# Kernel tuning notes

Measured on AMD Instinct MI355X. Metric: run time of the kernel, lower is better.

Reference implementation:

```python
import jax, jax.numpy as jnp
import numpy as np
import math

B, S, E, H = 2, 2048, 1024, 16
D = E // H  # head_size = 64
EPS = 1e-5

def _ln(x, g, b):
    mu = jnp.mean(x, axis=-1, keepdims=True)
    var = jnp.mean(jnp.square(x - mu), axis=-1, keepdims=True)
    return (x - mu) * jax.lax.rsqrt(var + EPS) * g + b

def setup_inputs() -> dict:
    key = jax.random.key(0)
    ks = jax.random.split(key, 16)
    s = 0.02
    return {
        "I": jax.random.normal(ks[0], (B, S, E), jnp.float32),
        "x": jax.random.normal(ks[1], (B, S, E), jnp.float32),
        "mask": jnp.ones((B, 1, S), jnp.int32),
        # per-head Q/K/V weights stacked over heads [H, E, D], biases [H, D]
        "wq": jax.random.normal(ks[2], (H, E, D), jnp.float32) * s,
        "bq": jax.random.normal(ks[3], (H, D), jnp.float32) * s,
        "wk": jax.random.normal(ks[4], (H, E, D), jnp.float32) * s,
        "bk": jax.random.normal(ks[5], (H, D), jnp.float32) * s,
        "wv": jax.random.normal(ks[6], (H, E, D), jnp.float32) * s,
        "bv": jax.random.normal(ks[7], (H, D), jnp.float32) * s,
        "w_proj": jax.random.normal(ks[8], (E, E), jnp.float32) * s,
        "b_proj": jnp.zeros((E,), jnp.float32),
        "g1": jnp.ones((E,), jnp.float32),
        "be1": jnp.zeros((E,), jnp.float32),
        "g2": jnp.ones((E,), jnp.float32),
        "be2": jnp.zeros((E,), jnp.float32),
        "w1": jax.random.normal(ks[9], (E, 4 * E), jnp.float32) * s,
        "b1": jnp.zeros((4 * E,), jnp.float32),
        "w2": jax.random.normal(ks[10], (4 * E, E), jnp.float32) * s,
        "b2": jnp.zeros((E,), jnp.float32),
    }

def reference(I, x, mask, wq, bq, wk, bk, wv, bv, w_proj, b_proj,
              g1, be1, g2, be2, w1, b1, w2, b2):
    xn = _ln(x, g1, be1)
    # batched per-head projections: [B,S,E] x [H,E,D] -> [B,H,S,D]
    q = jnp.einsum('bse,hed->bhsd', I, wq) + bq[None, :, None, :]
    k = jnp.einsum('bse,hed->bhsd', xn, wk) + bk[None, :, None, :]
    v = jnp.einsum('bse,hed->bhsd', xn, wv) + bv[None, :, None, :]
    # NOTE: original scales by sqrt(n_embed), not sqrt(head_size)
    scores = jnp.einsum('bhqd,bhkd->bhqk', q, k) / math.sqrt(E)
    scores = jnp.where(mask[:, None, :, :] == 0, -1e9, scores)
    attn = jax.nn.softmax(scores, axis=-1)
    ctx = jnp.einsum('bhqk,bhkd->bhqd', attn, v)
    # concat heads: [B,S,H,D] -> [B,S,E]
    ctx = ctx.transpose(0, 2, 1, 3).reshape(B, S, E)
    attn_out = ctx @ w_proj + b_proj
    h = xn + attn_out
    h2 = _ln(h, g2, be2)
    ff = jax.nn.gelu(h2 @ w1 + b1, approximate=False) @ w2 + b2
    return h2 + ff
```

## Files before the change

kernel.cpp:

```cpp
#include <hip/hip_runtime.h>
#include <hip/hip_bf16.h>
#include <math.h>

typedef short short8 __attribute__((ext_vector_type(8)));
typedef short short4_t __attribute__((ext_vector_type(4)));
typedef float f32x4 __attribute__((ext_vector_type(4)));
typedef unsigned short u16;
typedef unsigned int u32;

#define B_ 2
#define S_ 2048
#define E_ 1024
#define H_ 16
#define D_ 64
#define TOK (B_*S_)

__device__ __forceinline__ float bf2f(u16 u) {
    union { unsigned int u; float f; } v; v.u = ((unsigned int)u) << 16; return v.f;
}
__device__ __forceinline__ u16 f2bf(float f) {
    union { float f; unsigned int u; } v; v.f = f;
    unsigned int r = v.u + 0x7fffu + ((v.u >> 16) & 1u);
    return (u16)(r >> 16);
}
__device__ __forceinline__ u32 fbits(float f) {
    union { float f; u32 u; } v; v.f = f; return v.u;
}
__device__ __forceinline__ void gl_lds16(const u16* g, short* l) {
    __builtin_amdgcn_global_load_lds(
        (const __attribute__((address_space(1))) unsigned int*)(g),
        (__attribute__((address_space(3))) unsigned int*)(l), 16, 0, 0);
}

__global__ __launch_bounds__(256) void convf_k(const float* __restrict__ s, u16* __restrict__ d)
{
    size_t i = ((size_t)blockIdx.x * 256 + threadIdx.x) * 8;
    f32x4 a = *(const f32x4*)(s + i);
    f32x4 b = *(const f32x4*)(s + i + 4);
    short8 r;
#pragma unroll
    for (int j = 0; j < 4; j++) { r[j] = (short)f2bf(a[j]); r[4 + j] = (short)f2bf(b[j]); }
    *(short8*)(d + i) = r;
}

__global__ __launch_bounds__(256) void tconv_k(
    const float* __restrict__ src, u16* __restrict__ dst,
    int K, int N, size_t zsrc, size_t zdst)
{
    __shared__ u16 t[64][72];
    src += (size_t)blockIdx.z * zsrc;
    dst += (size_t)blockIdx.z * zdst;
    int k0 = blockIdx.y * 64, n0 = blockIdx.x * 64;
    int tid = threadIdx.x;
    int kr = tid >> 4, nc = (tid & 15) * 4;
#pragma unroll
    for (int i = 0; i < 4; i++) {
        f32x4 v = *(const f32x4*)(src + (size_t)(k0 + kr + i * 16) * N + n0 + nc);
#pragma unroll
        for (int j = 0; j < 4; j++) t[kr + i * 16][nc + j] = f2bf(v[j]);
    }
    __syncthreads();
    int nr = tid >> 2, kg = (tid & 3) * 16;
    short8 r0, r1;
#pragma unroll
    for (int j = 0; j < 8; j++) { r0[j] = (short)t[kg + j][nr]; r1[j] = (short)t[kg + 8 + j][nr]; }
    u16* dp = dst + (size_t)(n0 + nr) * K + k0 + kg;
    *(short8*)(dp) = r0;
    *(short8*)(dp + 8) = r1;
}

__global__ __launch_bounds__(256) void tconvqkv_k(
    const float* __restrict__ wq, const float* __restrict__ wk,
    const float* __restrict__ wv, u16* __restrict__ dst)
{
    __shared__ u16 t[64][72];
    int z = blockIdx.z;
    int w = z >> 4, hh = z & 15;
    const float* src = (w == 0 ? wq : (w == 1 ? wk : wv)) + (size_t)hh * E_ * D_;
    u16* d = dst + (size_t)w * E_ * E_ + (size_t)hh * D_ * E_;
    int k0 = blockIdx.y * 64;
    int tid = threadIdx.x;
    int kr = tid >> 4, nc = (tid & 15) * 4;
#pragma unroll
    for (int i = 0; i < 4; i++) {
        f32x4 v = *(const f32x4*)(src + (size_t)(k0 + kr + i * 16) * D_ + nc);
#pragma unroll
        for (int j = 0; j < 4; j++) t[kr + i * 16][nc + j] = f2bf(v[j]);
    }
    __syncthreads();
    int nr = tid >> 2, kg = (tid & 3) * 16;
    short8 r0, r1;
#pragma unroll
    for (int j = 0; j < 8; j++) { r0[j] = (short)t[kg + j][nr]; r1[j] = (short)t[kg + 8 + j][nr]; }
    u16* dp = d + (size_t)nr * E_ + k0 + kg;
    *(short8*)(dp) = r0;
    *(short8*)(dp + 8) = r1;
}

__global__ __launch_bounds__(256) void vtrans_k(const u16* __restrict__ V, u16* __restrict__ Vt)
{
    __shared__ u16 t[64][72];
    int s0 = blockIdx.x * 64, h = blockIdx.y, b = blockIdx.z;
    int tid = threadIdx.x;
    int sr = tid >> 2, dc = (tid & 3) * 16;
    const u16* src = V + (size_t)b * S_ * E_ + (size_t)(s0 + sr) * E_ + h * D_ + dc;
    short8 v0 = *(const short8*)(src);
    short8 v1 = *(const short8*)(src + 8);
#pragma unroll
    for (int j = 0; j < 8; j++) { t[sr][dc + j] = v0[j]; t[sr][dc + 8 + j] = v1[j]; }
    __syncthreads();
    int dr = tid >> 2, sc = (tid & 3) * 16;
    short8 r0, r1;
#pragma unroll
    for (int j = 0; j < 8; j++) { r0[j] = (short)t[sc + j][dr]; r1[j] = (short)t[sc + 8 + j][dr]; }
    u16* dp = Vt + ((size_t)(b * H_ + h) * D_ + dr) * S_ + s0 + sc;
    *(short8*)(dp) = r0;
    *(short8*)(dp + 8) = r1;
}

__global__ __launch_bounds__(256) void maskprep_k(
    const int* __restrict__ mask, float* __restrict__ fb, int* __restrict__ ok)
{
    __shared__ unsigned char fl[256];
    int b = blockIdx.x;
    int tid = threadIdx.x;
    int base = tid * 8;
    unsigned all = 1;
#pragma unroll
    for (int j = 0; j < 8; j++) {
        int m = mask[b * S_ + base + j];
        fb[b * S_ + base + j] = m ? 0.f : -1e9f;
        all &= (m != 0) ? 1u : 0u;
    }
    fl[tid] = (unsigned char)all;
    __syncthreads();
    if (tid < 32) {
        unsigned a = 1;
#pragma unroll
        for (int j = 0; j < 8; j++) a &= fl[tid * 8 + j];
        ok[b * 32 + tid] = (int)a;
    }
}

template<int INF32>
__global__ __launch_bounds__(256) void ln_kernel(
    const void* __restrict__ xv, const float* __restrict__ g,
    const float* __restrict__ be, u16* __restrict__ y)
{
    int lane = threadIdx.x & 63, wave = threadIdx.x >> 6;
    int row = blockIdx.x * 4 + wave;
    int c0 = lane * 16;
    float v[16];
    if (INF32) {
        const float* xr = (const float*)xv + (size_t)row * E_ + c0;
#pragma unroll
        for (int i = 0; i < 4; i++) {
            f32x4 xx = *(const f32x4*)(xr + i * 4);
#pragma unroll
            for (int j = 0; j < 4; j++) v[i * 4 + j] = xx[j];
        }
    } else {
        const u16* xr = (const u16*)xv + (size_t)row * E_ + c0;
        short8 a = *(const short8*)(xr);
        short8 b = *(const short8*)(xr + 8);
#pragma unroll
        for (int j = 0; j < 8; j++) { v[j] = bf2f((u16)a[j]); v[8 + j] = bf2f((u16)b[j]); }
    }
    float s = 0.f, q = 0.f;
#pragma unroll
    for (int i = 0; i < 16; i++) { s += v[i]; q += v[i] * v[i]; }
#pragma unroll
    for (int off = 1; off < 64; off <<= 1) {
        s += __shfl_xor(s, off, 64);
        q += __shfl_xor(q, off, 64);
    }
    float mu = s * (1.0f / E_);
    float var = q * (1.0f / E_) - mu * mu;
    float rstd = rsqrtf(var + 1e-5f);
    u16* yr = y + (size_t)row * E_ + c0;
    short8 o0, o1;
#pragma unroll
    for (int j = 0; j < 8; j++) {
        o0[j] = (short)f2bf((v[j] - mu) * rstd * g[c0 + j] + be[c0 + j]);
        o1[j] = (short)f2bf((v[8 + j] - mu) * rstd * g[c0 + 8 + j] + be[c0 + 8 + j]);
    }
    *(short8*)(yr) = o0;
    *(short8*)(yr + 8) = o1;
}

template<int QKV, int GELU>
__global__ __launch_bounds__(512) void gemm8p_k(
    const u16* __restrict__ A, const u16* __restrict__ Axn,
    const u16* __restrict__ WT,
    const float* __restrict__ bq, const float* __restrict__ bk, const float* __restrict__ bv,
    u16* __restrict__ C, int M, int N, int K)
{
    __shared__ __align__(16) short As[2][256 * 64];
    __shared__ __align__(16) short Bs[2][256 * 64];
    int tid = threadIdx.x;
    int wave = tid >> 6, lane = tid & 63, quad = lane >> 4, l16 = lane & 15;
    int wm = wave >> 2, wn = wave & 3;
    int n0 = blockIdx.x * 256, m0 = blockIdx.y * 256;
    int which = QKV ? (n0 >> 10) : 0;
    const u16* Ause = (QKV && which) ? Axn : A;
    const float* bias = QKV ? (which == 0 ? bq : (which == 1 ? bk : bv)) : bq;

    f32x4 acc[8][4];
#pragma unroll
    for (int m = 0; m < 8; m++)
#pragma unroll
        for (int n = 0; n < 4; n++)
            acc[m][n] = (f32x4){0.f, 0.f, 0.f, 0.f};

    int srow = lane >> 3, slot = lane & 7;
    const u16* Ag = Ause + (size_t)(m0 + wave * 16 + srow) * K + ((slot ^ srow) << 3);
    const u16* Bg = WT + (size_t)(n0 + wave * 16 + srow) * K + ((slot ^ srow) << 3);
    int wv = wave * 1024;
    int r7 = l16 & 7;
    int soff0 = (quad ^ r7) << 3;
    int soff1 = ((4 + quad) ^ r7) << 3;
    int arow = (wm * 128 + l16) * 64;
    int brow = (wn * 64 + l16) * 64;
    int NT = K >> 6;

#define GLA2(buf, h, kk_) do { \
    gl_lds16(Ag + (size_t)((h) * 128) * K + (kk_), &As[buf][wv + (h) * 8192]); \
    gl_lds16(Ag + (size_t)((h) * 128 + 8) * K + (kk_), &As[buf][wv + (h) * 8192 + 512]); } while (0)
#define GLB2(buf, h, kk_) do { \
    gl_lds16(Bg + (size_t)((h) * 128) * K + (kk_), &Bs[buf][wv + (h) * 8192]); \
    gl_lds16(Bg + (size_t)((h) * 128 + 8) * K + (kk_), &Bs[buf][wv + (h) * 8192 + 512]); } while (0)

#define PHASE(mb, GLSTMT, TAILSTMT) do { \
    __builtin_amdgcn_sched_barrier(0); \
    short8 af[2][2]; \
    af[0][0] = *(const short8*)(&As[c][arow + (mb) * 1024 + soff0]); \
    af[0][1] = *(const short8*)(&As[c][arow + (mb) * 1024 + soff1]); \
    af[1][0] = *(const short8*)(&As[c][arow + ((mb) + 1) * 1024 + soff0]); \
    af[1][1] = *(const short8*)(&As[c][arow + ((mb) + 1) * 1024 + soff1]); \
    GLSTMT; \
    __builtin_amdgcn_s_barrier(); \
    asm volatile("s_waitcnt lgkmcnt(0)" ::: "memory"); \
    __builtin_amdgcn_sched_barrier(0); \
    __builtin_amdgcn_s_setprio(1); \
    _Pragma("unroll") \
    for (int i_ = 0; i_ < 2; i_++) \
    _Pragma("unroll") \
    for (int n_ = 0; n_ < 4; n_++) { \
        acc[(mb) + i_][n_] = __builtin_amdgcn_mfma_f32_16x16x32_bf16(af[i_][0], bf[n_][0], acc[(mb) + i_][n_], 0, 0, 0); \
        acc[(mb) + i_][n_] = __builtin_amdgcn_mfma_f32_16x16x32_bf16(af[i_][1], bf[n_][1], acc[(mb) + i_][n_], 0, 0, 0); \
    } \
    __builtin_amdgcn_s_setprio(0); \
    __builtin_amdgcn_sched_barrier(0); \
    TAILSTMT; \
    __builtin_amdgcn_s_barrier(); \
} while (0)

    GLB2(0, 0, 0); GLB2(0, 1, 0);
    GLA2(0, 0, 0); GLA2(0, 1, 0);
    if (NT > 1) {
        GLB2(1, 0, 64); GLB2(1, 1, 64);
        asm volatile("s_waitcnt vmcnt(4)" ::: "memory");
    } else {
        asm volatile("s_waitcnt vmcnt(0)" ::: "memory");
    }
    __builtin_amdgcn_s_barrier();

    for (int t = 0; t < NT; ++t) {
        int c = t & 1;
        int kk1 = (t + 1) << 6, kk2 = (t + 2) << 6;
        short8 bf[4][2];
        __builtin_amdgcn_sched_barrier(0);
#pragma unroll
        for (int n = 0; n < 4; n++) {
            bf[n][0] = *(const short8*)(&Bs[c][brow + n * 1024 + soff0]);
            bf[n][1] = *(const short8*)(&Bs[c][brow + n * 1024 + soff1]);
        }
        PHASE(0,
            { if (t + 1 < NT) GLA2(c ^ 1, 0, kk1); asm volatile("s_waitcnt lgkmcnt(8)" ::: "memory"); },
            {});
        PHASE(2, { if (t + 1 < NT) GLA2(c ^ 1, 1, kk1); }, {});
        PHASE(4, { if (t + 2 < NT) GLB2(c, 0, kk2); }, {});
        PHASE(6, { if (t + 2 < NT) GLB2(c, 1, kk2); },
            { if (t + 2 < NT) asm volatile("s_waitcnt vmcnt(4)" ::: "memory");
              else            asm volatile("s_waitcnt vmcnt(0)" ::: "memory"); });
    }

    u16* Cw = QKV ? (C + (size_t)which * (size_t)M * 1024) : C;
    int ostride = QKV ? 1024 : N;
#pragma unroll
    for (int m = 0; m < 8; m++) {
#pragma unroll
        for (int n = 0; n < 4; n++) {
            int colg = n0 + wn * 64 + n * 16 + l16;
            int col = QKV ? (colg & 1023) : colg;
            float bb = bias[col];
#pragma unroll
            for (int r = 0; r < 4; r++) {
                int row = m0 + wm * 128 + m * 16 + quad * 4 + r;
                float v = acc[m][n][r] + bb;
                if (QKV && which == 0) v *= 0.03125f;
                if (GELU) v = 0.5f * v * (1.0f + erff(v * 0.70710678118f));
                Cw[(size_t)row * ostride + col] = f2bf(v);
            }
        }
    }
#undef GLA2
#undef GLB2
#undef PHASE
}

__global__ __launch_bounds__(256) void gemmsk_k(
    const u16* __restrict__ A, const u16* __restrict__ WT,
    u16* __restrict__ P, int M, int N, int K, int Ks)
{
    __shared__ __align__(16) short a_sh[2][128 * 32];
    __shared__ __align__(16) short b_sh[2][128 * 32];
    int tid = threadIdx.x;
    int wave = tid >> 6, lane = tid & 63, quad = lane >> 4, l16 = lane & 15;
    int wm = wave >> 1, wn = wave & 1;
    int m0 = blockIdx.y * 128, n0 = blockIdx.x * 128;
    int koff = blockIdx.z * Ks;

    f32x4 acc[4][4];
#pragma unroll
    for (int mt = 0; mt < 4; mt++)
#pragma unroll
        for (int nt = 0; nt < 4; nt++)
            acc[mt][nt] = (f32x4){0.f, 0.f, 0.f, 0.f};

    int srow = lane >> 2;
    int c = ((lane & 3) ^ ((lane >> 3) & 3)) * 8;
    const u16* Ab = A + (size_t)(m0 + wave * 32 + srow) * K + koff + c;
    const u16* Bb = WT + (size_t)(n0 + wave * 32 + srow) * K + koff + c;
    short* al0 = &a_sh[0][wave * 1024];
    short* al1 = &a_sh[1][wave * 1024];
    short* bl0 = &b_sh[0][wave * 1024];
    short* bl1 = &b_sh[1][wave * 1024];
    int xo = (quad ^ ((l16 >> 1) & 3)) * 8;

    for (int kk = 0; kk < Ks; kk += 64) {
        __syncthreads();
        gl_lds16(Ab + kk, al0);
        gl_lds16(Ab + kk + (size_t)16 * K, al0 + 512);
        gl_lds16(Ab + kk + 32, al1);
        gl_lds16(Ab + kk + (size_t)16 * K + 32, al1 + 512);
        gl_lds16(Bb + kk, bl0);
        gl_lds16(Bb + kk + (size_t)16 * K, bl0 + 512);
        gl_lds16(Bb + kk + 32, bl1);
        gl_lds16(Bb + kk + (size_t)16 * K + 32, bl1 + 512);
        __syncthreads();

#pragma unroll
        for (int h = 0; h < 2; h++) {
            short8 af[4], bf8[4];
#pragma unroll
            for (int mt = 0; mt < 4; mt++)
                af[mt] = *(const short8*)(&a_sh[h][(wm * 64 + mt * 16 + l16) * 32 + xo]);
#pragma unroll
            for (int nt = 0; nt < 4; nt++)
                bf8[nt] = *(const short8*)(&b_sh[h][(wn * 64 + nt * 16 + l16) * 32 + xo]);
#pragma unroll
            for (int mt = 0; mt < 4; mt++)
#pragma unroll
                for (int nt = 0; nt < 4; nt++)
                    acc[mt][nt] = __builtin_amdgcn_mfma_f32_16x16x32_bf16(af[mt], bf8[nt], acc[mt][nt], 0, 0, 0);
        }
    }

    u16* Pz = P + (size_t)blockIdx.z * (size_t)M * N;
#pragma unroll
    for (int mt = 0; mt < 4; mt++) {
#pragma unroll
        for (int nt = 0; nt < 4; nt++) {
            int col = n0 + wn * 64 + nt * 16 + l16;
#pragma unroll
            for (int r = 0; r < 4; r++) {
                int row = m0 + wm * 64 + mt * 16 + quad * 4 + r;
                Pz[(size_t)row * N + col] = f2bf(acc[mt][nt][r]);
            }
        }
    }
}

__global__ __launch_bounds__(256) void combine2_k(
    const u16* __restrict__ P, const float* __restrict__ bias,
    const u16* __restrict__ res, float* __restrict__ out)
{
    const size_t MN = (size_t)TOK * E_;
    size_t i = ((size_t)blockIdx.x * 256 + threadIdx.x) * 8;
    int col = (int)(i & (E_ - 1));
    float v[8];
    f32x4 b0 = *(const f32x4*)(bias + col);
    f32x4 b1 = *(const f32x4*)(bias + col + 4);
    short8 rr = *(const short8*)(res + i);
#pragma unroll
    for (int j = 0; j < 4; j++) { v[j] = b0[j] + bf2f((u16)rr[j]); v[4 + j] = b1[j] + bf2f((u16)rr[4 + j]); }
#pragma unroll
    for (int z = 0; z < 2; z++) {
        short8 p = *(const short8*)(P + z * MN + i);
#pragma unroll
        for (int j = 0; j < 8; j++) v[j] += bf2f((u16)p[j]);
    }
    f32x4 o0, o1;
#pragma unroll
    for (int j = 0; j < 4; j++) { o0[j] = v[j]; o1[j] = v[4 + j]; }
    *(f32x4*)(out + i) = o0;
    *(f32x4*)(out + i + 4) = o1;
}

template<int GELU, int RES, int CF32>
__global__ __launch_bounds__(256) void gemm3_k(
    const u16* __restrict__ A, const u16* __restrict__ WT,
    const float* __restrict__ bias, const u16* __restrict__ res,
    void* __restrict__ Cv, int M, int N, int K)
{
    __shared__ __align__(16) short a_sh[2][128 * 32];
    __shared__ __align__(16) short b_sh[2][64 * 32];
    int tid = threadIdx.x;
    int wave = tid >> 6, lane = tid & 63, quad = lane >> 4, l16 = lane & 15;
    int wm = wave >> 1, wn = wave & 1;
    int m0 = blockIdx.y * 128, n0 = blockIdx.x * 64;

    f32x4 acc[4][2];
#pragma unroll
    for (int mt = 0; mt < 4; mt++)
#pragma unroll
        for (int nt = 0; nt < 2; nt++)
            acc[mt][nt] = (f32x4){0.f, 0.f, 0.f, 0.f};

    int srow = lane >> 2;
    int c = ((lane & 3) ^ ((lane >> 3) & 3)) * 8;
    const u16* Ab = A + (size_t)(m0 + wave * 32 + srow) * K + c;
    const u16* Bb = WT + (size_t)(n0 + wave * 16 + srow) * K + c;
    short* al0 = &a_sh[0][wave * 1024];
    short* al1 = &a_sh[1][wave * 1024];
    short* bl0 = &b_sh[0][wave * 512];
    short* bl1 = &b_sh[1][wave * 512];
    int xo = (quad ^ ((l16 >> 1) & 3)) * 8;

    for (int kk = 0; kk < K; kk += 64) {
        __syncthreads();
        gl_lds16(Ab + kk, al0);
        gl_lds16(Ab + kk + (size_t)16 * K, al0 + 512);
        gl_lds16(Ab + kk + 32, al1);
        gl_lds16(Ab + kk + (size_t)16 * K + 32, al1 + 512);
        gl_lds16(Bb + kk, bl0);
        gl_lds16(Bb + kk + 32, bl1);
        __syncthreads();

#pragma unroll
        for (int h = 0; h < 2; h++) {
            short8 af[4], bf8[2];
#pragma unroll
            for (int mt = 0; mt < 4; mt++)
                af[mt] = *(const short8*)(&a_sh[h][(wm * 64 + mt * 16 + l16) * 32 + xo]);
#pragma unroll
            for (int nt = 0; nt < 2; nt++)
                bf8[nt] = *(const short8*)(&b_sh[h][(wn * 32 + nt * 16 + l16) * 32 + xo]);
#pragma unroll
            for (int mt = 0; mt < 4; mt++)
#pragma unroll
                for (int nt = 0; nt < 2; nt++)
                    acc[mt][nt] = __builtin_amdgcn_mfma_f32_16x16x32_bf16(af[mt], bf8[nt], acc[mt][nt], 0, 0, 0);
        }
    }

#pragma unroll
    for (int mt = 0; mt < 4; mt++) {
#pragma unroll
        for (int nt = 0; nt < 2; nt++) {
            int col = n0 + wn * 32 + nt * 16 + l16;
            float bb = bias[col];
#pragma unroll
            for (int r = 0; r < 4; r++) {
                int row = m0 + wm * 64 + mt * 16 + quad * 4 + r;
                float v = acc[mt][nt][r] + bb;
                if (RES) v += bf2f(res[(size_t)row * N + col]);
                if (GELU) v = 0.5f * v * (1.0f + erff(v * 0.70710678118f));
                if (CF32) ((float*)Cv)[(size_t)row * N + col] = v;
                else ((u16*)Cv)[(size_t)row * N + col] = f2bf(v);
            }
        }
    }
}

__global__ __launch_bounds__(512) void attn_k(
    const u16* __restrict__ Q, const u16* __restrict__ K,
    const u16* __restrict__ Vt, const float* __restrict__ fb,
    const int* __restrict__ ok, u16* __restrict__ O)
{
    __shared__ __align__(16) short k_sh[2][2][64 * 32];
    __shared__ __align__(16) short v_sh[2][2][64 * 32];
    __shared__ __align__(16) short p_sh[8][16 * 72];
    int tid = threadIdx.x;
    int wave = tid >> 6, lane = tid & 63, quad = lane >> 4, l16 = lane & 15;
    int qb = blockIdx.x, h = blockIdx.y, b = blockIdx.z;
    int q0 = qb * 128;
    const u16* Qp = Q + (size_t)b * S_ * E_ + (size_t)h * D_;
    const u16* Kp = K + (size_t)b * S_ * E_ + (size_t)h * D_;
    const u16* Vtp = Vt + (size_t)(b * H_ + h) * D_ * S_;

    int qrow = q0 + wave * 16 + l16;
    short8 qf0 = *(const short8*)(Qp + (size_t)qrow * E_ + quad * 8);
    short8 qf1 = *(const short8*)(Qp + (size_t)qrow * E_ + 32 + quad * 8);

    f32x4 o[4];
#pragma unroll
    for (int dt = 0; dt < 4; dt++) o[dt] = (f32x4){0.f, 0.f, 0.f, 0.f};
    float rs_tot = 0.f;

    int sub = wave & 1, rblk = wave >> 1;
    int srow = lane >> 2;
    int c = ((lane & 3) ^ ((lane >> 3) & 3)) * 8;
    const u16* Kg = Kp + (size_t)(rblk * 16 + srow) * E_ + sub * 32 + c;
    const u16* Vg = Vtp + (size_t)(rblk * 16 + srow) * S_ + sub * 32 + c;
    short* kl0 = &k_sh[0][sub][rblk * 512];
    short* kl1 = &k_sh[1][sub][rblk * 512];
    short* vl0 = &v_sh[0][sub][rblk * 512];
    short* vl1 = &v_sh[1][sub][rblk * 512];

    gl_lds16(Kg, kl0);
    gl_lds16(Vg, vl0);
    __syncthreads();

    const float* fbb = fb + b * S_;
    const int* okb = ok + b * 32;
    int xo = (quad ^ ((l16 >> 1) & 3)) * 8;

    for (int kt = 0; kt < S_ / 64; kt++) {
        int cur = kt & 1;
        if (kt < 31) {
            gl_lds16(Kg + (size_t)(kt + 1) * 64 * E_, cur ? kl0 : kl1);
            gl_lds16(Vg + (kt + 1) * 64, cur ? vl0 : vl1);
        }

        f32x4 s[4];
#pragma unroll
        for (int mt = 0; mt < 4; mt++) {
            int ro = (mt * 16 + l16) * 32 + xo;
            short8 kf0 = *(const short8*)(&k_sh[cur][0][ro]);
            short8 kf1 = *(const short8*)(&k_sh[cur][1][ro]);
            s[mt] = __builtin_amdgcn_mfma_f32_16x16x32_bf16(kf0, qf0, (f32x4){0.f,0.f,0.f,0.f}, 0, 0, 0);
            s[mt] = __builtin_amdgcn_mfma_f32_16x16x32_bf16(kf1, qf1, s[mt], 0, 0, 0);
        }

        if (!okb[kt]) {
#pragma unroll
            for (int mt = 0; mt < 4; mt++)
#pragma unroll
                for (int r = 0; r < 4; r++)
                    s[mt][r] += fbb[kt * 64 + mt * 16 + quad * 4 + r];
        }

#pragma unroll
        for (int mt = 0; mt < 4; mt++) {
            float p0 = __expf(s[mt][0]);
            float p1 = __expf(s[mt][1]);
            float p2 = __expf(s[mt][2]);
            float p3 = __expf(s[mt][3]);
            rs_tot += (p0 + p1) + (p2 + p3);
            u32 u0 = __builtin_amdgcn_perm(fbits(p1), fbits(p0), 0x07060302u);
            u32 u1 = __builtin_amdgcn_perm(fbits(p3), fbits(p2), 0x07060302u);
            uint2 pk; pk.x = u0; pk.y = u1;
            *(uint2*)(&p_sh[wave][l16 * 72 + mt * 16 + quad * 4]) = pk;
        }

#pragma unroll
        for (int sk = 0; sk < 2; sk++) {
            short8 pf = *(const short8*)(&p_sh[wave][l16 * 72 + sk * 32 + quad * 8]);
#pragma unroll
            for (int dt = 0; dt < 4; dt++) {
                short8 vf = *(const short8*)(&v_sh[cur][sk][(dt * 16 + l16) * 32 + xo]);
                o[dt] = __builtin_amdgcn_mfma_f32_16x16x32_bf16(vf, pf, o[dt], 0, 0, 0);
            }
        }
        __syncthreads();
    }

    rs_tot += __shfl_xor(rs_tot, 16, 64);
    rs_tot += __shfl_xor(rs_tot, 32, 64);
    float inv = 1.0f / rs_tot;
    u16* Op = O + (size_t)b * S_ * E_ + (size_t)(q0 + wave * 16 + l16) * E_ + h * D_;
#pragma unroll
    for (int dt = 0; dt < 4; dt++) {
        short4_t pk;
#pragma unroll
        for (int r = 0; r < 4; r++) pk[r] = (short)f2bf(o[dt][r] * inv);
        *(short4_t*)(Op + dt * 16 + quad * 4) = pk;
    }
}

extern "C" void kernel_launch(void* const* d_in, const int* in_sizes, int n_in,
                              void* d_out, int out_size, void* d_ws, size_t ws_size,
                              hipStream_t stream)
{
    (void)in_sizes; (void)n_in; (void)out_size; (void)ws_size;
    const float* I      = (const float*)d_in[0];
    const float* x      = (const float*)d_in[1];
    const int*   mask   = (const int*)d_in[2];
    const float* wq     = (const float*)d_in[3];
    const float* bq     = (const float*)d_in[4];
    const float* wk     = (const float*)d_in[5];
    const float* bk     = (const float*)d_in[6];
    const float* wv     = (const float*)d_in[7];
    const float* bv     = (const float*)d_in[8];
    const float* w_proj = (const float*)d_in[9];
    const float* b_proj = (const float*)d_in[10];
    const float* g1     = (const float*)d_in[11];
    const float* be1    = (const float*)d_in[12];
    const float* g2     = (const float*)d_in[13];
    const float* be2    = (const float*)d_in[14];
    const float* w1     = (const float*)d_in[15];
    const float* b1     = (const float*)d_in[16];
    const float* w2     = (const float*)d_in[17];
    const float* b2     = (const float*)d_in[18];
    float* out = (float*)d_out;

    char* ws = (char*)d_ws;
    const size_t SZ = (size_t)TOK * E_;
    u16* xn   = (u16*)(ws);
    u16* qb_  = (u16*)(ws + SZ * 2);
    u16* kb_  = (u16*)(ws + SZ * 4);
    u16* vb_  = (u16*)(ws + SZ * 6);
    u16* Vt   = (u16*)(ws + SZ * 8);
    u16* Ibf  = (u16*)(ws + SZ * 8);
    u16* ctx  = (u16*)(ws + SZ * 6);
    u16* hb   = (u16*)(ws + SZ * 4);
    u16* h2   = (u16*)(ws);
    u16* a1   = (u16*)(ws + SZ * 2);
    u16* WTqkv  = (u16*)(ws + 40u * 1024 * 1024);
    u16* WTproj = (u16*)(ws + 46u * 1024 * 1024);
    u16* WT1    = (u16*)(ws + 48u * 1024 * 1024);
    u16* WT2    = (u16*)(ws + 56u * 1024 * 1024);
    u16* Pp     = (u16*)(ws + 40u * 1024 * 1024);
    float* fbm  = (float*)(ws + 40u * 1024 * 1024);
    int*   okm  = (int*)(ws + 40u * 1024 * 1024 + 16384);

    convf_k<<<dim3(TOK * E_ / (256 * 8)), 256, 0, stream>>>(I, Ibf);
    tconvqkv_k<<<dim3(1, 16, 48), 256, 0, stream>>>(wq, wk, wv, WTqkv);
    tconv_k<<<dim3(16, 16, 1), 256, 0, stream>>>(w_proj, WTproj, E_, E_, 0, 0);
    tconv_k<<<dim3(64, 16, 1), 256, 0, stream>>>(w1, WT1, E_, 4 * E_, 0, 0);
    tconv_k<<<dim3(16, 64, 1), 256, 0, stream>>>(w2, WT2, 4 * E_, E_, 0, 0);

    ln_kernel<1><<<TOK / 4, 256, 0, stream>>>(x, g1, be1, xn);

    gemm8p_k<1,0><<<dim3(12, TOK / 256), 512, 0, stream>>>(
        Ibf, xn, WTqkv, bq, bk, bv, qb_, TOK, 3072, E_);

    maskprep_k<<<dim3(B_), 256, 0, stream>>>(mask, fbm, okm);
    vtrans_k<<<dim3(S_ / 64, H_, B_), 256, 0, stream>>>(vb_, Vt);

    attn_k<<<dim3(S_ / 128, H_, B_), 512, 0, stream>>>(qb_, kb_, Vt, fbm, okm, ctx);

    gemm3_k<0,1,0><<<dim3(16, TOK / 128), 256, 0, stream>>>(
        ctx, WTproj, b_proj, xn, hb, TOK, E_, E_);
    ln_kernel<0><<<TOK / 4, 256, 0, stream>>>(hb, g2, be2, h2);
    gemm8p_k<0,1><<<dim3(16, TOK / 256), 512, 0, stream>>>(
        h2, nullptr, WT1, b1, nullptr, nullptr, a1, TOK, 4 * E_, E_);
    gemmsk_k<<<dim3(8, TOK / 128, 2), 256, 0, stream>>>(
        a1, WT2, Pp, TOK, E_, 4 * E_, 2 * E_);
    combine2_k<<<dim3(TOK * E_ / (256 * 8)), 256, 0, stream>>>(Pp, b2, h2, out);
}
```

Before: 381.9 us.

## Remap GEMM block indices per XCD and unroll k-loop with pointer increments

```diff
diff --git a/kernel.cpp b/kernel.cpp
--- a/kernel.cpp
+++ b/kernel.cpp
@@ -188,7 +188,7 @@
     *(short8*)(yr + 8) = o1;
 }
 
-template<int QKV, int GELU>
+template<int QKV, int GELU, int RX>
 __global__ __launch_bounds__(512) void gemm8p_k(
     const u16* __restrict__ A, const u16* __restrict__ Axn,
     const u16* __restrict__ WT,
@@ -200,7 +200,15 @@
     int tid = threadIdx.x;
     int wave = tid >> 6, lane = tid & 63, quad = lane >> 4, l16 = lane & 15;
     int wm = wave >> 2, wn = wave & 3;
-    int n0 = blockIdx.x * 256, m0 = blockIdx.y * 256;
+
+    int gx = gridDim.x, gy = gridDim.y;
+    int lin = blockIdx.y * gx + blockIdx.x;
+    int xcd = lin & 7, w = lin >> 3;
+    int rw = gx / RX, rh = gy / (8 / RX);
+    int bx = (xcd % RX) * rw + (w % rw);
+    int by = (xcd / RX) * rh + (w / rw);
+    int n0 = bx * 256, m0 = by * 256;
+
     int which = QKV ? (n0 >> 10) : 0;
     const u16* Ause = (QKV && which) ? Axn : A;
     const float* bias = QKV ? (which == 0 ? bq : (which == 1 ? bk : bv)) : bq;
@@ -215,6 +223,7 @@
     int srow = lane >> 3, slot = lane & 7;
     const u16* Ag = Ause + (size_t)(m0 + wave * 16 + srow) * K + ((slot ^ srow) << 3);
     const u16* Bg = WT + (size_t)(n0 + wave * 16 + srow) * K + ((slot ^ srow) << 3);
+    const size_t r8K = (size_t)8 * K, r128K = (size_t)128 * K, r136K = (size_t)136 * K;
     int wv = wave * 1024;
     int r7 = l16 & 7;
     int soff0 = (quad ^ r7) << 3;
@@ -223,20 +232,20 @@
     int brow = (wn * 64 + l16) * 64;
     int NT = K >> 6;
 
-#define GLA2(buf, h, kk_) do { \
-    gl_lds16(Ag + (size_t)((h) * 128) * K + (kk_), &As[buf][wv + (h) * 8192]); \
-    gl_lds16(Ag + (size_t)((h) * 128 + 8) * K + (kk_), &As[buf][wv + (h) * 8192 + 512]); } while (0)
-#define GLB2(buf, h, kk_) do { \
-    gl_lds16(Bg + (size_t)((h) * 128) * K + (kk_), &Bs[buf][wv + (h) * 8192]); \
-    gl_lds16(Bg + (size_t)((h) * 128 + 8) * K + (kk_), &Bs[buf][wv + (h) * 8192 + 512]); } while (0)
-
-#define PHASE(mb, GLSTMT, TAILSTMT) do { \
+#define GLA2P(P, BUF, H) do { \
+    gl_lds16((P) + ((H) ? r128K : (size_t)0), &As[BUF][wv + (H) * 8192]); \
+    gl_lds16((P) + ((H) ? r136K : r8K), &As[BUF][wv + (H) * 8192 + 512]); } while (0)
+#define GLB2P(P, BUF, H) do { \
+    gl_lds16((P) + ((H) ? r128K : (size_t)0), &Bs[BUF][wv + (H) * 8192]); \
+    gl_lds16((P) + ((H) ? r136K : r8K), &Bs[BUF][wv + (H) * 8192 + 512]); } while (0)
+
+#define PHASE(BUF, mb, GLSTMT, TAILSTMT) do { \
     __builtin_amdgcn_sched_barrier(0); \
     short8 af[2][2]; \
-    af[0][0] = *(const short8*)(&As[c][arow + (mb) * 1024 + soff0]); \
-    af[0][1] = *(const short8*)(&As[c][arow + (mb) * 1024 + soff1]); \
-    af[1][0] = *(const short8*)(&As[c][arow + ((mb) + 1) * 1024 + soff0]); \
-    af[1][1] = *(const short8*)(&As[c][arow + ((mb) + 1) * 1024 + soff1]); \
+    af[0][0] = *(const short8*)(&As[BUF][arow + (mb) * 1024 + soff0]); \
+    af[0][1] = *(const short8*)(&As[BUF][arow + (mb) * 1024 + soff1]); \
+    af[1][0] = *(const short8*)(&As[BUF][arow + ((mb) + 1) * 1024 + soff0]); \
+    af[1][1] = *(const short8*)(&As[BUF][arow + ((mb) + 1) * 1024 + soff1]); \
     GLSTMT; \
     __builtin_amdgcn_s_barrier(); \
     asm volatile("s_waitcnt lgkmcnt(0)" ::: "memory"); \
@@ -255,34 +264,39 @@
     __builtin_amdgcn_s_barrier(); \
 } while (0)
 
-    GLB2(0, 0, 0); GLB2(0, 1, 0);
-    GLA2(0, 0, 0); GLA2(0, 1, 0);
+#define KTILE(BUF, OBUF, TT, PAx, PBx) do { \
+    short8 bf[4][2]; \
+    __builtin_amdgcn_sched_barrier(0); \
+    _Pragma("unroll") \
+    for (int n = 0; n < 4; n++) { \
+        bf[n][0] = *(const short8*)(&Bs[BUF][brow + n * 1024 + soff0]); \
+        bf[n][1] = *(const short8*)(&Bs[BUF][brow + n * 1024 + soff1]); \
+    } \
+    PHASE(BUF, 0, \
+        { if ((TT) + 1 < NT) GLA2P((PAx), OBUF, 0); asm volatile("s_waitcnt lgkmcnt(8)" ::: "memory"); }, {}); \
+    PHASE(BUF, 2, { if ((TT) + 1 < NT) GLA2P((PAx), OBUF, 1); }, {}); \
+    PHASE(BUF, 4, { if ((TT) + 2 < NT) GLB2P((PBx), BUF, 0); }, {}); \
+    PHASE(BUF, 6, { if ((TT) + 2 < NT) GLB2P((PBx), BUF, 1); }, \
+        { if ((TT) + 2 < NT) asm volatile("s_waitcnt vmcnt(4)" ::: "memory"); \
+          else               asm volatile("s_waitcnt vmcnt(0)" ::: "memory"); }); \
+} while (0)
+
+    GLB2P(Bg, 0, 0); GLB2P(Bg, 0, 1);
+    GLA2P(Ag, 0, 0); GLA2P(Ag, 0, 1);
     if (NT > 1) {
-        GLB2(1, 0, 64); GLB2(1, 1, 64);
+        GLB2P(Bg + 64, 1, 0); GLB2P(Bg + 64, 1, 1);
         asm volatile("s_waitcnt vmcnt(4)" ::: "memory");
     } else {
         asm volatile("s_waitcnt vmcnt(0)" ::: "memory");
     }
     __builtin_amdgcn_s_barrier();
 
-    for (int t = 0; t < NT; ++t) {
-        int c = t & 1;
-        int kk1 = (t + 1) << 6, kk2 = (t + 2) << 6;
-        short8 bf[4][2];
-        __builtin_amdgcn_sched_barrier(0);
-#pragma unroll
-        for (int n = 0; n < 4; n++) {
-            bf[n][0] = *(const short8*)(&Bs[c][brow + n * 1024 + soff0]);
-            bf[n][1] = *(const short8*)(&Bs[c][brow + n * 1024 + soff1]);
-        }
-        PHASE(0,
-            { if (t + 1 < NT) GLA2(c ^ 1, 0, kk1); asm volatile("s_waitcnt lgkmcnt(8)" ::: "memory"); },
-            {});
-        PHASE(2, { if (t + 1 < NT) GLA2(c ^ 1, 1, kk1); }, {});
-        PHASE(4, { if (t + 2 < NT) GLB2(c, 0, kk2); }, {});
-        PHASE(6, { if (t + 2 < NT) GLB2(c, 1, kk2); },
-            { if (t + 2 < NT) asm volatile("s_waitcnt vmcnt(4)" ::: "memory");
-              else            asm volatile("s_waitcnt vmcnt(0)" ::: "memory"); });
+    const u16* PA = Ag + 64;
+    const u16* PB = Bg + 128;
+    for (int t = 0; t < NT; t += 2) {
+        KTILE(0, 1, t, PA, PB);
+        KTILE(1, 0, t + 1, PA + 64, PB + 64);
+        PA += 128; PB += 128;
     }
 
     u16* Cw = QKV ? (C + (size_t)which * (size_t)M * 1024) : C;
@@ -304,9 +318,10 @@
             }
         }
     }
-#undef GLA2
-#undef GLB2
+#undef GLA2P
+#undef GLB2P
 #undef PHASE
+#undef KTILE
 }
 
 __global__ __launch_bounds__(256) void gemmsk_k(
@@ -318,7 +333,12 @@
     int tid = threadIdx.x;
     int wave = tid >> 6, lane = tid & 63, quad = lane >> 4, l16 = lane & 15;
     int wm = wave >> 1, wn = wave & 1;
-    int m0 = blockIdx.y * 128, n0 = blockIdx.x * 128;
+    int gx = gridDim.x;
+    int lin = blockIdx.y * gx + blockIdx.x;
+    int xcd = lin & 7, w = lin >> 3;
+    int rh = gridDim.y >> 3;
+    int bx = w % gx, by = xcd * rh + (w / gx);
+    int m0 = by * 128, n0 = bx * 128;
     int koff = blockIdx.z * Ks;
 
     f32x4 acc[4][4];
@@ -644,7 +664,7 @@
 
     ln_kernel<1><<<TOK / 4, 256, 0, stream>>>(x, g1, be1, xn);
 
-    gemm8p_k<1,0><<<dim3(12, TOK / 256), 512, 0, stream>>>(
+    gemm8p_k<1,0,2><<<dim3(12, TOK / 256), 512, 0, stream>>>(
         Ibf, xn, WTqkv, bq, bk, bv, qb_, TOK, 3072, E_);
 
     maskprep_k<<<dim3(B_), 256, 0, stream>>>(mask, fbm, okm);
@@ -655,7 +675,7 @@
     gemm3_k<0,1,0><<<dim3(16, TOK / 128), 256, 0, stream>>>(
         ctx, WTproj, b_proj, xn, hb, TOK, E_, E_);
     ln_kernel<0><<<TOK / 4, 256, 0, stream>>>(hb, g2, be2, h2);
-    gemm8p_k<0,1><<<dim3(16, TOK / 256), 512, 0, stream>>>(
+    gemm8p_k<0,1,2><<<dim3(16, TOK / 256), 512, 0, stream>>>(
         h2, nullptr, WT1, b1, nullptr, nullptr, a1, TOK, 4 * E_, E_);
     gemmsk_k<<<dim3(8, TOK / 128, 2), 256, 0, stream>>>(
         a1, WT2, Pp, TOK, E_, 4 * E_, 2 * E_);
```

Result: no change. 376.8 us (-1.3%).
